# Optimization experiments

Hardware: AMD Instinct MI355X
Metric: run time of the kernel (lower is better)

The kernel has to match this reference:

```python
import jax, jax.numpy as jnp
import numpy as np

N_NODES = 100000
FIELD_DIM = 128
EMBED_DIM = 64
N_EDGES = 3200000
BATCH = 8192
NUM_FIELDS = 2


def setup_inputs() -> dict:
    key = jax.random.key(0)
    k1, k2, k3, k4 = jax.random.split(key, 4)
    features = jax.random.normal(k1, (N_NODES, FIELD_DIM), dtype=jnp.float32)
    edge_index = jax.random.randint(k2, (2, N_EDGES), 0, N_NODES, dtype=jnp.int32)
    # GCNConv linear weight (Glorot-ish scale) and bias
    W = jax.random.normal(k3, (FIELD_DIM, EMBED_DIM), dtype=jnp.float32) * (1.0 / np.sqrt(FIELD_DIM))
    bias = jnp.zeros((EMBED_DIM,), dtype=jnp.float32)
    x = jax.random.randint(k4, (BATCH, NUM_FIELDS), 0, N_NODES, dtype=jnp.int32)
    return {"features": features, "edge_index": edge_index, "W": W, "bias": bias, "x": x}


def reference(features, edge_index, W, bias, x):
    # GCNConv: out = D^{-1/2} (A + I) D^{-1/2} (X W) + b, then gather rows by x.
    n = features.shape[0]
    loop = jnp.arange(n, dtype=edge_index.dtype)
    src = jnp.concatenate([edge_index[0], loop])  # [E + N]
    dst = jnp.concatenate([edge_index[1], loop])  # [E + N]
    # degree (with self-loops) per destination node; >= 1 so rsqrt is safe
    deg = jax.ops.segment_sum(jnp.ones_like(dst, dtype=features.dtype), dst, num_segments=n)
    dinv = jax.lax.rsqrt(deg)
    norm = dinv[src] * dinv[dst]  # [E + N]
    h = features @ W  # [N, EMBED_DIM]
    msgs = h[src] * norm[:, None]  # gather + scale
    out = jax.ops.segment_sum(msgs, dst, num_segments=n) + bias  # [N, EMBED_DIM]
    return out[x]  # [BATCH, NUM_FIELDS, EMBED_DIM]
```

## Files before the change

kernel.cpp:

```cpp
#include <hip/hip_runtime.h>

#define N_NODES   100000
#define FIELD_DIM 128
#define EMBED_DIM 64
#define N_EDGES   3200000
#define NX        16384

#define NRANGE    4
#define RN        25000
#define RNH       12500
#define NSLICE    64
#define SLICE_E   (N_EDGES / NSLICE)
#define FILLB     (N_EDGES / 4 / 256)
#define GEMMB     ((N_NODES + 63) / 64)

typedef short  bf16x8 __attribute__((ext_vector_type(8)));
typedef float  f32x4  __attribute__((ext_vector_type(4)));

__device__ __forceinline__ unsigned short f2bf(float x) {
    unsigned u = __float_as_uint(x);
    u += 0x7FFF + ((u >> 16) & 1);
    return (unsigned short)(u >> 16);
}
__device__ __forceinline__ float bf2f(unsigned short b) {
    return __uint_as_float(((unsigned)b) << 16);
}
__device__ __forceinline__ unsigned pk2(float lo, float hi) {
    return (unsigned)f2bf(lo) | ((unsigned)f2bf(hi) << 16);
}

__global__ void k_zero(float4* __restrict__ z4) {
    int i = blockIdx.x * blockDim.x + threadIdx.x;
    if (i < 784) z4[i] = make_float4(0.f, 0.f, 0.f, 0.f);
}

__global__ void k_init(const int* __restrict__ x, unsigned int* __restrict__ bits,
                       const float* __restrict__ W, unsigned short* __restrict__ Wt) {
    int b = blockIdx.x;
    if (b < 64) {
        int i = b * 256 + threadIdx.x;
        int v = x[i];
        atomicOr(&bits[v >> 5], 1u << (v & 31));
    } else {
        for (int i = threadIdx.x; i < FIELD_DIM * EMBED_DIM; i += 256) {
            int k = i >> 6, c = i & 63;
            Wt[c * FIELD_DIM + k] = f2bf(W[i]);
        }
    }
}

__global__ __launch_bounds__(256) void k_hist(const int* __restrict__ dst,
                                              unsigned int* __restrict__ partial32) {
    __shared__ unsigned int hist[RNH];
    int tid = threadIdx.x;
    int q = blockIdx.x & 3, s = blockIdx.x >> 2;
    for (int i = tid; i < RNH; i += 256) hist[i] = 0;
    __syncthreads();
    int lo = q * RN;
    const int4* dp = (const int4*)(dst + s * SLICE_E);
    for (int i = tid; i < SLICE_E / 4; i += 256) {
        int4 d = dp[i];
        int a;
        a = d.x - lo; if ((unsigned)a < RN) atomicAdd(&hist[a >> 1], 1u << ((a & 1) << 4));
        a = d.y - lo; if ((unsigned)a < RN) atomicAdd(&hist[a >> 1], 1u << ((a & 1) << 4));
        a = d.z - lo; if ((unsigned)a < RN) atomicAdd(&hist[a >> 1], 1u << ((a & 1) << 4));
        a = d.w - lo; if ((unsigned)a < RN) atomicAdd(&hist[a >> 1], 1u << ((a & 1) << 4));
    }
    __syncthreads();
    unsigned int* po = partial32 + (size_t)blockIdx.x * RNH;
    for (int i = tid; i < RNH; i += 256) po[i] = hist[i];
}

__global__ __launch_bounds__(256) void k_reduce(const unsigned int* __restrict__ partial32,
                                                const unsigned int* __restrict__ bits,
                                                int* __restrict__ cnt,
                                                float* __restrict__ dinv,
                                                int* __restrict__ nlist,
                                                int* __restrict__ inv,
                                                int* __restrict__ off,
                                                int* __restrict__ cur,
                                                unsigned long long* __restrict__ counters) {
    __shared__ int wtot[4], wedge[4], ptot[4], pedge[4];
    __shared__ unsigned int baseN, baseE;
    int tid = threadIdx.x;
    int v = blockIdx.x * 256 + tid;
    bool inb = (v < N_NODES);
    int vc = inb ? v : (N_NODES - 1);
    int q = vc / RN, loc = vc - q * RN;
    int i2 = loc >> 1, sh = (loc & 1) << 4;
    const unsigned int* p = partial32 + (size_t)q * RNH + i2;
    int c = 0;
#pragma unroll
    for (int sb = 0; sb < 4; ++sb) {
        unsigned int vals[16];
#pragma unroll
        for (int s = 0; s < 16; ++s) vals[s] = p[(size_t)(sb * 16 + s) * (NRANGE * RNH)];
#pragma unroll
        for (int s = 0; s < 16; ++s) c += (int)((vals[s] >> sh) & 0xFFFFu);
    }
    if (inb) {
        cnt[v] = c;
        dinv[v] = rsqrtf((float)c + 1.0f);
    }
    bool fl = inb && ((bits[v >> 5] >> (v & 31)) & 1u);
    int lane = tid & 63;
    int w = tid >> 6;
    unsigned long long mask = __ballot(fl);
    int cc = fl ? c : 0;
    int incl = cc;
#pragma unroll
    for (int o = 1; o < 64; o <<= 1) {
        int t = __shfl_up(incl, o);
        if (lane >= o) incl += t;
    }
    if (lane == 63) { wtot[w] = __popcll(mask); wedge[w] = incl; }
    int myi = __popcll(mask & ((1ull << lane) - 1));
    int excl = incl - cc;
    __syncthreads();
    if (tid == 0) {
        int t0 = wtot[0], t1 = wtot[1], t2 = wtot[2], t3 = wtot[3];
        int e0 = wedge[0], e1 = wedge[1], e2 = wedge[2], e3 = wedge[3];
        ptot[0] = 0; ptot[1] = t0; ptot[2] = t0 + t1; ptot[3] = t0 + t1 + t2;
        pedge[0] = 0; pedge[1] = e0; pedge[2] = e0 + e1; pedge[3] = e0 + e1 + e2;
        int bt = t0 + t1 + t2 + t3;
        int be = e0 + e1 + e2 + e3;
        if (bt > 0) {
            unsigned long long add = ((unsigned long long)(unsigned)be << 32) |
                                     (unsigned long long)(unsigned)bt;
            unsigned long long old = atomicAdd(counters, add);
            baseN = (unsigned)(old & 0xFFFFFFFFull);
            baseE = (unsigned)(old >> 32);
        } else {
            baseN = 0; baseE = 0;
        }
    }
    __syncthreads();
    if (fl) {
        int i = (int)baseN + ptot[w] + myi;
        int o = (int)baseE + pedge[w] + excl;
        nlist[i] = v;
        inv[v] = i;
        off[v] = o;
        cur[v] = o;
    }
}

__global__ __launch_bounds__(256) void k_fillgemm(const int* __restrict__ src,
                                                  const int* __restrict__ dst,
                                                  const unsigned int* __restrict__ bits,
                                                  int* __restrict__ cur,
                                                  int* __restrict__ elist,
                                                  const float* __restrict__ F,
                                                  const unsigned short* __restrict__ Wt,
                                                  unsigned short* __restrict__ h) {
    if (blockIdx.x < FILLB) {
        int i = blockIdx.x * 256 + threadIdx.x;
        int4 d4 = ((const int4*)dst)[i];
        int4 s4 = ((const int4*)src)[i];
#define FILL1(dd, ss) if ((bits[(unsigned)(dd) >> 5] >> ((dd) & 31)) & 1u) \
        { int p = atomicAdd(&cur[dd], 1); elist[p] = ss; }
        FILL1(d4.x, s4.x)
        FILL1(d4.y, s4.y)
        FILL1(d4.z, s4.z)
        FILL1(d4.w, s4.w)
#undef FILL1
        return;
    }
    int gb = blockIdx.x - FILLB;
    int tid = threadIdx.x;
    int wave = tid >> 6, lane = tid & 63;
    int l15 = lane & 15, kg = lane >> 4;

    const char* wb = (const char*)Wt;
    bf16x8 bfrag[4][4];
#pragma unroll
    for (int cb = 0; cb < 4; ++cb)
#pragma unroll
        for (int ks = 0; ks < 4; ++ks)
            bfrag[cb][ks] = *(const bf16x8*)(wb + (cb * 16 + l15) * 256 + ks * 64 + kg * 16);

    int row = gb * 64 + wave * 16 + l15;
    int rowc = min(row, N_NODES - 1);
    const float4* F4 = (const float4*)(F + (size_t)rowc * FIELD_DIM + kg * 8);

    f32x4 acc[4];
#pragma unroll
    for (int cb = 0; cb < 4; ++cb) acc[cb] = (f32x4){0.f, 0.f, 0.f, 0.f};

#pragma unroll
    for (int ks = 0; ks < 4; ++ks) {
        float4 fa = F4[ks * 8];
        float4 fb = F4[ks * 8 + 1];
        union { bf16x8 v; unsigned u[4]; } af;
        af.u[0] = pk2(fa.x, fa.y);
        af.u[1] = pk2(fa.z, fa.w);
        af.u[2] = pk2(fb.x, fb.y);
        af.u[3] = pk2(fb.z, fb.w);
#pragma unroll
        for (int cb = 0; cb < 4; ++cb)
            acc[cb] = __builtin_amdgcn_mfma_f32_16x16x32_bf16(af.v, bfrag[cb][ks],
                                                              acc[cb], 0, 0, 0);
    }
    int rbase = gb * 64 + wave * 16 + kg * 4;
#pragma unroll
    for (int r = 0; r < 4; ++r) {
        int orow = rbase + r;
        if (orow < N_NODES) {
            unsigned short* hp = h + (size_t)orow * 64 + l15;
#pragma unroll
            for (int cb = 0; cb < 4; ++cb) hp[cb * 16] = f2bf(acc[cb][r]);
        }
    }
}

__global__ __launch_bounds__(256) void k_pull(const int* __restrict__ nlist,
                                              const int* __restrict__ counters,
                                              const int* __restrict__ cnt,
                                              const int* __restrict__ off,
                                              const int* __restrict__ elist,
                                              const unsigned short* __restrict__ h,
                                              const float* __restrict__ dinv,
                                              const float* __restrict__ bias,
                                              float* __restrict__ accc) {
    int t = blockIdx.x * blockDim.x + threadIdx.x;
    int wid = t >> 6;
    int lane = t & 63;
    if (wid >= counters[0]) return;
    int v = nlist[wid];
    float dvd = dinv[v];
    int deg = cnt[v];
    int base = off[v];
    float acc = bf2f(h[(size_t)v * 64 + lane]) * (dvd * dvd) + bias[lane];
    float acc2 = 0.f;
    int j = 0;
    for (; j + 7 < deg; j += 8) {
        int s0 = elist[base + j + 0];
        int s1 = elist[base + j + 1];
        int s2 = elist[base + j + 2];
        int s3 = elist[base + j + 3];
        int s4 = elist[base + j + 4];
        int s5 = elist[base + j + 5];
        int s6 = elist[base + j + 6];
        int s7 = elist[base + j + 7];
        float v0 = bf2f(h[(size_t)s0 * 64 + lane]);
        float v1 = bf2f(h[(size_t)s1 * 64 + lane]);
        float v2 = bf2f(h[(size_t)s2 * 64 + lane]);
        float v3 = bf2f(h[(size_t)s3 * 64 + lane]);
        float v4 = bf2f(h[(size_t)s4 * 64 + lane]);
        float v5 = bf2f(h[(size_t)s5 * 64 + lane]);
        float v6 = bf2f(h[(size_t)s6 * 64 + lane]);
        float v7 = bf2f(h[(size_t)s7 * 64 + lane]);
        float n0 = dinv[s0], n1 = dinv[s1], n2 = dinv[s2], n3 = dinv[s3];
        float n4 = dinv[s4], n5 = dinv[s5], n6 = dinv[s6], n7 = dinv[s7];
        acc  += v0 * (n0 * dvd);
        acc2 += v1 * (n1 * dvd);
        acc  += v2 * (n2 * dvd);
        acc2 += v3 * (n3 * dvd);
        acc  += v4 * (n4 * dvd);
        acc2 += v5 * (n5 * dvd);
        acc  += v6 * (n6 * dvd);
        acc2 += v7 * (n7 * dvd);
    }
    for (; j < deg; ++j) {
        int s0 = elist[base + j];
        acc += bf2f(h[(size_t)s0 * 64 + lane]) * (dinv[s0] * dvd);
    }
    accc[(size_t)wid * 64 + lane] = acc + acc2;
}

__global__ void k_gather(const int* __restrict__ x,
                         const int* __restrict__ inv,
                         const float* __restrict__ accc,
                         float* __restrict__ out) {
    int g = blockIdx.x * blockDim.x + threadIdx.x;
    if (g >= NX * 64) return;
    int v = x[g >> 6];
    out[g] = accc[(size_t)inv[v] * 64 + (g & 63)];
}

extern "C" void kernel_launch(void* const* d_in, const int* in_sizes, int n_in,
                              void* d_out, int out_size, void* d_ws, size_t ws_size,
                              hipStream_t stream) {
    const float* features = (const float*)d_in[0];
    const int*   edge     = (const int*)d_in[1];
    const float* W        = (const float*)d_in[2];
    const float* bias     = (const float*)d_in[3];
    const int*   x        = (const int*)d_in[4];
    float* out = (float*)d_out;

    char* ws = (char*)d_ws;
    unsigned short* h16      = (unsigned short*)(ws);
    unsigned int*   partial32= (unsigned int*)(ws + 12800000);
    int*            elist    = (int*)(ws + 12800000);
    float*          accc     = (float*)(ws + 25600000);
    int*            cnt      = (int*)  (ws + 29794304);
    float*          dinv     = (float*)(ws + 30194304);
    int*            off      = (int*)  (ws + 30594304);
    int*            inv      = (int*)  (ws + 30994304);
    int*            nlist    = (int*)  (ws + 31394304);
    int*            cur      = (int*)  (ws + 31459840);
    unsigned long long* counters = (unsigned long long*)(ws + 31859840);
    unsigned int*   bits     = (unsigned int*) (ws + 31859872);
    unsigned short* Wt       = (unsigned short*)(ws + 31872384);

    const int* esrc = edge;
    const int* edst = edge + N_EDGES;

    k_zero    <<<4, 256, 0, stream>>>((float4*)(ws + 31859840));
    k_init    <<<65, 256, 0, stream>>>(x, bits, W, Wt);
    k_hist    <<<NRANGE * NSLICE, 256, 0, stream>>>(edst, partial32);
    k_reduce  <<<(N_NODES + 255) / 256, 256, 0, stream>>>(partial32, bits, cnt, dinv,
                                                          nlist, inv, off, cur, counters);
    k_fillgemm<<<FILLB + GEMMB, 256, 0, stream>>>(esrc, edst, bits, cur, elist,
                                                  features, Wt, h16);
    k_pull    <<<(NX * 64 + 255) / 256, 256, 0, stream>>>(nlist, (const int*)counters,
                                                          cnt, off, elist, h16, dinv,
                                                          bias, accc);
    k_gather  <<<(NX * 64 + 255) / 256, 256, 0, stream>>>(x, inv, accc, out);
}
```

Baseline: 122.4 us.

## Co-schedule GEMM with histogram kernel and pad fill cursors per node

Moves the feature GEMM out of the edge-fill kernel and interleaves its blocks with the degree histogram blocks, one histogram block per seven. The fill kernel becomes standalone, and its per-node atomic cursors are spaced 64 bytes apart to reduce contention on shared cache lines. The trade-offs are a larger workspace footprint for the cursor array and the loss of the earlier overlap between the GEMM and the fill.

```diff
diff --git a/kernel.cpp b/kernel.cpp
--- a/kernel.cpp
+++ b/kernel.cpp
@@ -11,8 +11,9 @@
 #define RNH       12500
 #define NSLICE    64
 #define SLICE_E   (N_EDGES / NSLICE)
+#define HISTB     (NRANGE * NSLICE)
+#define GEMMB     ((N_NODES + 63) / 64)
 #define FILLB     (N_EDGES / 4 / 256)
-#define GEMMB     ((N_NODES + 63) / 64)
 
 typedef short  bf16x8 __attribute__((ext_vector_type(8)));
 typedef float  f32x4  __attribute__((ext_vector_type(4)));
@@ -49,26 +50,79 @@
     }
 }
 
-__global__ __launch_bounds__(256) void k_hist(const int* __restrict__ dst,
-                                              unsigned int* __restrict__ partial32) {
+__global__ __launch_bounds__(256) void k_histgemm(const int* __restrict__ dst,
+                                                  unsigned int* __restrict__ partial32,
+                                                  const float* __restrict__ F,
+                                                  const unsigned short* __restrict__ Wt,
+                                                  unsigned short* __restrict__ h) {
     __shared__ unsigned int hist[RNH];
+    int b = blockIdx.x;
     int tid = threadIdx.x;
-    int q = blockIdx.x & 3, s = blockIdx.x >> 2;
-    for (int i = tid; i < RNH; i += 256) hist[i] = 0;
-    __syncthreads();
-    int lo = q * RN;
-    const int4* dp = (const int4*)(dst + s * SLICE_E);
-    for (int i = tid; i < SLICE_E / 4; i += 256) {
-        int4 d = dp[i];
-        int a;
-        a = d.x - lo; if ((unsigned)a < RN) atomicAdd(&hist[a >> 1], 1u << ((a & 1) << 4));
-        a = d.y - lo; if ((unsigned)a < RN) atomicAdd(&hist[a >> 1], 1u << ((a & 1) << 4));
-        a = d.z - lo; if ((unsigned)a < RN) atomicAdd(&hist[a >> 1], 1u << ((a & 1) << 4));
-        a = d.w - lo; if ((unsigned)a < RN) atomicAdd(&hist[a >> 1], 1u << ((a & 1) << 4));
-    }
-    __syncthreads();
-    unsigned int* po = partial32 + (size_t)blockIdx.x * RNH;
-    for (int i = tid; i < RNH; i += 256) po[i] = hist[i];
+    bool ish = ((b % 7) == 0) && (b / 7 < HISTB);
+    if (ish) {
+        int hid = b / 7;
+        int q = hid & 3, s = hid >> 2;
+        for (int i = tid; i < RNH; i += 256) hist[i] = 0;
+        __syncthreads();
+        int lo = q * RN;
+        const int4* dp = (const int4*)(dst + s * SLICE_E);
+        for (int i = tid; i < SLICE_E / 4; i += 256) {
+            int4 d = dp[i];
+            int a;
+            a = d.x - lo; if ((unsigned)a < RN) atomicAdd(&hist[a >> 1], 1u << ((a & 1) << 4));
+            a = d.y - lo; if ((unsigned)a < RN) atomicAdd(&hist[a >> 1], 1u << ((a & 1) << 4));
+            a = d.z - lo; if ((unsigned)a < RN) atomicAdd(&hist[a >> 1], 1u << ((a & 1) << 4));
+            a = d.w - lo; if ((unsigned)a < RN) atomicAdd(&hist[a >> 1], 1u << ((a & 1) << 4));
+        }
+        __syncthreads();
+        unsigned int* po = partial32 + (size_t)hid * RNH;
+        for (int i = tid; i < RNH; i += 256) po[i] = hist[i];
+        return;
+    }
+    int gb = b - min((b + 6) / 7, HISTB);
+    int wave = tid >> 6, lane = tid & 63;
+    int l15 = lane & 15, kg = lane >> 4;
+
+    const char* wb = (const char*)Wt;
+    bf16x8 bfrag[4][4];
+#pragma unroll
+    for (int cb = 0; cb < 4; ++cb)
+#pragma unroll
+        for (int ks = 0; ks < 4; ++ks)
+            bfrag[cb][ks] = *(const bf16x8*)(wb + (cb * 16 + l15) * 256 + ks * 64 + kg * 16);
+
+    int row = gb * 64 + wave * 16 + l15;
+    int rowc = min(row, N_NODES - 1);
+    const float4* F4 = (const float4*)(F + (size_t)rowc * FIELD_DIM + kg * 8);
+
+    f32x4 acc[4];
+#pragma unroll
+    for (int cb = 0; cb < 4; ++cb) acc[cb] = (f32x4){0.f, 0.f, 0.f, 0.f};
+
+#pragma unroll
+    for (int ks = 0; ks < 4; ++ks) {
+        float4 fa = F4[ks * 8];
+        float4 fb = F4[ks * 8 + 1];
+        union { bf16x8 v; unsigned u[4]; } af;
+        af.u[0] = pk2(fa.x, fa.y);
+        af.u[1] = pk2(fa.z, fa.w);
+        af.u[2] = pk2(fb.x, fb.y);
+        af.u[3] = pk2(fb.z, fb.w);
+#pragma unroll
+        for (int cb = 0; cb < 4; ++cb)
+            acc[cb] = __builtin_amdgcn_mfma_f32_16x16x32_bf16(af.v, bfrag[cb][ks],
+                                                              acc[cb], 0, 0, 0);
+    }
+    int rbase = gb * 64 + wave * 16 + kg * 4;
+#pragma unroll
+    for (int r = 0; r < 4; ++r) {
+        int orow = rbase + r;
+        if (orow < N_NODES) {
+            unsigned short* hp = h + (size_t)orow * 64 + l15;
+#pragma unroll
+            for (int cb = 0; cb < 4; ++cb) hp[cb * 16] = f2bf(acc[cb][r]);
+        }
+    }
 }
 
 __global__ __launch_bounds__(256) void k_reduce(const unsigned int* __restrict__ partial32,
@@ -78,7 +132,7 @@
                                                 int* __restrict__ nlist,
                                                 int* __restrict__ inv,
                                                 int* __restrict__ off,
-                                                int* __restrict__ cur,
+                                                int* __restrict__ cur16,
                                                 unsigned long long* __restrict__ counters) {
     __shared__ int wtot[4], wedge[4], ptot[4], pedge[4];
     __shared__ unsigned int baseN, baseE;
@@ -141,76 +195,25 @@
         nlist[i] = v;
         inv[v] = i;
         off[v] = o;
-        cur[v] = o;
-    }
-}
-
-__global__ __launch_bounds__(256) void k_fillgemm(const int* __restrict__ src,
-                                                  const int* __restrict__ dst,
-                                                  const unsigned int* __restrict__ bits,
-                                                  int* __restrict__ cur,
-                                                  int* __restrict__ elist,
-                                                  const float* __restrict__ F,
-                                                  const unsigned short* __restrict__ Wt,
-                                                  unsigned short* __restrict__ h) {
-    if (blockIdx.x < FILLB) {
-        int i = blockIdx.x * 256 + threadIdx.x;
-        int4 d4 = ((const int4*)dst)[i];
-        int4 s4 = ((const int4*)src)[i];
+        cur16[v << 4] = o;
+    }
+}
+
+__global__ __launch_bounds__(256) void k_fill(const int* __restrict__ src,
+                                              const int* __restrict__ dst,
+                                              const unsigned int* __restrict__ bits,
+                                              int* __restrict__ cur16,
+                                              int* __restrict__ elist) {
+    int i = blockIdx.x * 256 + threadIdx.x;
+    int4 d4 = ((const int4*)dst)[i];
+    int4 s4 = ((const int4*)src)[i];
 #define FILL1(dd, ss) if ((bits[(unsigned)(dd) >> 5] >> ((dd) & 31)) & 1u) \
-        { int p = atomicAdd(&cur[dd], 1); elist[p] = ss; }
-        FILL1(d4.x, s4.x)
-        FILL1(d4.y, s4.y)
-        FILL1(d4.z, s4.z)
-        FILL1(d4.w, s4.w)
+    { int p = atomicAdd(&cur16[(dd) << 4], 1); elist[p] = ss; }
+    FILL1(d4.x, s4.x)
+    FILL1(d4.y, s4.y)
+    FILL1(d4.z, s4.z)
+    FILL1(d4.w, s4.w)
 #undef FILL1
-        return;
-    }
-    int gb = blockIdx.x - FILLB;
-    int tid = threadIdx.x;
-    int wave = tid >> 6, lane = tid & 63;
-    int l15 = lane & 15, kg = lane >> 4;
-
-    const char* wb = (const char*)Wt;
-    bf16x8 bfrag[4][4];
-#pragma unroll
-    for (int cb = 0; cb < 4; ++cb)
-#pragma unroll
-        for (int ks = 0; ks < 4; ++ks)
-            bfrag[cb][ks] = *(const bf16x8*)(wb + (cb * 16 + l15) * 256 + ks * 64 + kg * 16);
-
-    int row = gb * 64 + wave * 16 + l15;
-    int rowc = min(row, N_NODES - 1);
-    const float4* F4 = (const float4*)(F + (size_t)rowc * FIELD_DIM + kg * 8);
-
-    f32x4 acc[4];
-#pragma unroll
-    for (int cb = 0; cb < 4; ++cb) acc[cb] = (f32x4){0.f, 0.f, 0.f, 0.f};
-
-#pragma unroll
-    for (int ks = 0; ks < 4; ++ks) {
-        float4 fa = F4[ks * 8];
-        float4 fb = F4[ks * 8 + 1];
-        union { bf16x8 v; unsigned u[4]; } af;
-        af.u[0] = pk2(fa.x, fa.y);
-        af.u[1] = pk2(fa.z, fa.w);
-        af.u[2] = pk2(fb.x, fb.y);
-        af.u[3] = pk2(fb.z, fb.w);
-#pragma unroll
-        for (int cb = 0; cb < 4; ++cb)
-            acc[cb] = __builtin_amdgcn_mfma_f32_16x16x32_bf16(af.v, bfrag[cb][ks],
-                                                              acc[cb], 0, 0, 0);
-    }
-    int rbase = gb * 64 + wave * 16 + kg * 4;
-#pragma unroll
-    for (int r = 0; r < 4; ++r) {
-        int orow = rbase + r;
-        if (orow < N_NODES) {
-            unsigned short* hp = h + (size_t)orow * 64 + l15;
-#pragma unroll
-            for (int cb = 0; cb < 4; ++cb) hp[cb * 16] = f2bf(acc[cb][r]);
-        }
-    }
 }
 
 __global__ __launch_bounds__(256) void k_pull(const int* __restrict__ nlist,
@@ -298,21 +301,20 @@
     int*            off      = (int*)  (ws + 30594304);
     int*            inv      = (int*)  (ws + 30994304);
     int*            nlist    = (int*)  (ws + 31394304);
-    int*            cur      = (int*)  (ws + 31459840);
-    unsigned long long* counters = (unsigned long long*)(ws + 31859840);
-    unsigned int*   bits     = (unsigned int*) (ws + 31859872);
-    unsigned short* Wt       = (unsigned short*)(ws + 31872384);
+    unsigned long long* counters = (unsigned long long*)(ws + 31459840);
+    unsigned int*   bits     = (unsigned int*) (ws + 31459872);
+    unsigned short* Wt       = (unsigned short*)(ws + 31472384);
+    int*            cur16    = (int*)  (ws + 31488768);
 
     const int* esrc = edge;
     const int* edst = edge + N_EDGES;
 
-    k_zero    <<<4, 256, 0, stream>>>((float4*)(ws + 31859840));
+    k_zero    <<<4, 256, 0, stream>>>((float4*)(ws + 31459840));
     k_init    <<<65, 256, 0, stream>>>(x, bits, W, Wt);
-    k_hist    <<<NRANGE * NSLICE, 256, 0, stream>>>(edst, partial32);
+    k_histgemm<<<HISTB + GEMMB, 256, 0, stream>>>(edst, partial32, features, Wt, h16);
     k_reduce  <<<(N_NODES + 255) / 256, 256, 0, stream>>>(partial32, bits, cnt, dinv,
-                                                          nlist, inv, off, cur, counters);
-    k_fillgemm<<<FILLB + GEMMB, 256, 0, stream>>>(esrc, edst, bits, cur, elist,
-                                                  features, Wt, h16);
+                                                          nlist, inv, off, cur16, counters);
+    k_fill    <<<FILLB, 256, 0, stream>>>(esrc, edst, bits, cur16, elist);
     k_pull    <<<(NX * 64 + 255) / 256, 256, 0, stream>>>(nlist, (const int*)counters,
                                                           cnt, off, elist, h16, dinv,
                                                           bias, accc);
```

New measurement: 121.3 us. About the same (-0.9%).

## Interleave fill and GEMM blocks, pad atomic cursors, widen histogram slicing

Applied to the files above, without the earlier changes.

The edge-histogram kernel now uses 125 slices instead of 64, launching more blocks, and each thread issues five vectorized loads before its shared-memory atomics. The fill/GEMM kernel interleaves one GEMM block between every two fill blocks instead of placing all GEMM blocks after the fill blocks, so compute-bound and atomic-bound work share the GPU. The per-node fill cursors are spread to one per 64-byte stride to cut atomic contention on shared cache lines. The workspace layout is moved to fit the larger partial-histogram buffer and the padded cursor array, which uses more memory and more reduce reads.

```diff
diff --git a/kernel.cpp b/kernel.cpp
--- a/kernel.cpp
+++ b/kernel.cpp
@@ -9,10 +9,11 @@
 #define NRANGE    4
 #define RN        25000
 #define RNH       12500
-#define NSLICE    64
+#define NSLICE    125
 #define SLICE_E   (N_EDGES / NSLICE)
+#define HISTB     (NRANGE * NSLICE)
+#define GEMMB     ((N_NODES + 63) / 64)
 #define FILLB     (N_EDGES / 4 / 256)
-#define GEMMB     ((N_NODES + 63) / 64)
 
 typedef short  bf16x8 __attribute__((ext_vector_type(8)));
 typedef float  f32x4  __attribute__((ext_vector_type(4)));
@@ -58,13 +59,19 @@
     __syncthreads();
     int lo = q * RN;
     const int4* dp = (const int4*)(dst + s * SLICE_E);
-    for (int i = tid; i < SLICE_E / 4; i += 256) {
-        int4 d = dp[i];
-        int a;
-        a = d.x - lo; if ((unsigned)a < RN) atomicAdd(&hist[a >> 1], 1u << ((a & 1) << 4));
-        a = d.y - lo; if ((unsigned)a < RN) atomicAdd(&hist[a >> 1], 1u << ((a & 1) << 4));
-        a = d.z - lo; if ((unsigned)a < RN) atomicAdd(&hist[a >> 1], 1u << ((a & 1) << 4));
-        a = d.w - lo; if ((unsigned)a < RN) atomicAdd(&hist[a >> 1], 1u << ((a & 1) << 4));
+#pragma unroll
+    for (int bt = 0; bt < 5; ++bt) {
+        int4 d[5];
+#pragma unroll
+        for (int u = 0; u < 5; ++u) d[u] = dp[tid + 256 * (bt * 5 + u)];
+#pragma unroll
+        for (int u = 0; u < 5; ++u) {
+            int a;
+            a = d[u].x - lo; if ((unsigned)a < RN) atomicAdd(&hist[a >> 1], 1u << ((a & 1) << 4));
+            a = d[u].y - lo; if ((unsigned)a < RN) atomicAdd(&hist[a >> 1], 1u << ((a & 1) << 4));
+            a = d[u].z - lo; if ((unsigned)a < RN) atomicAdd(&hist[a >> 1], 1u << ((a & 1) << 4));
+            a = d[u].w - lo; if ((unsigned)a < RN) atomicAdd(&hist[a >> 1], 1u << ((a & 1) << 4));
+        }
     }
     __syncthreads();
     unsigned int* po = partial32 + (size_t)blockIdx.x * RNH;
@@ -78,7 +85,7 @@
                                                 int* __restrict__ nlist,
                                                 int* __restrict__ inv,
                                                 int* __restrict__ off,
-                                                int* __restrict__ cur,
+                                                int* __restrict__ cur16,
                                                 unsigned long long* __restrict__ counters) {
     __shared__ int wtot[4], wedge[4], ptot[4], pedge[4];
     __shared__ unsigned int baseN, baseE;
@@ -91,12 +98,12 @@
     const unsigned int* p = partial32 + (size_t)q * RNH + i2;
     int c = 0;
 #pragma unroll
-    for (int sb = 0; sb < 4; ++sb) {
-        unsigned int vals[16];
-#pragma unroll
-        for (int s = 0; s < 16; ++s) vals[s] = p[(size_t)(sb * 16 + s) * (NRANGE * RNH)];
-#pragma unroll
-        for (int s = 0; s < 16; ++s) c += (int)((vals[s] >> sh) & 0xFFFFu);
+    for (int sb = 0; sb < 5; ++sb) {
+        unsigned int vals[25];
+#pragma unroll
+        for (int s = 0; s < 25; ++s) vals[s] = p[(size_t)(sb * 25 + s) * (NRANGE * RNH)];
+#pragma unroll
+        for (int s = 0; s < 25; ++s) c += (int)((vals[s] >> sh) & 0xFFFFu);
     }
     if (inb) {
         cnt[v] = c;
@@ -141,24 +148,28 @@
         nlist[i] = v;
         inv[v] = i;
         off[v] = o;
-        cur[v] = o;
+        cur16[v << 4] = o;
     }
 }
 
 __global__ __launch_bounds__(256) void k_fillgemm(const int* __restrict__ src,
                                                   const int* __restrict__ dst,
                                                   const unsigned int* __restrict__ bits,
-                                                  int* __restrict__ cur,
+                                                  int* __restrict__ cur16,
                                                   int* __restrict__ elist,
                                                   const float* __restrict__ F,
                                                   const unsigned short* __restrict__ Wt,
                                                   unsigned short* __restrict__ h) {
-    if (blockIdx.x < FILLB) {
-        int i = blockIdx.x * 256 + threadIdx.x;
+    int b = blockIdx.x;
+    int tid = threadIdx.x;
+    bool isg = ((b % 3) == 0) && (b / 3 < GEMMB);
+    if (!isg) {
+        int fb = b - min(b / 3 + 1, GEMMB);
+        int i = fb * 256 + tid;
         int4 d4 = ((const int4*)dst)[i];
         int4 s4 = ((const int4*)src)[i];
 #define FILL1(dd, ss) if ((bits[(unsigned)(dd) >> 5] >> ((dd) & 31)) & 1u) \
-        { int p = atomicAdd(&cur[dd], 1); elist[p] = ss; }
+        { int p = atomicAdd(&cur16[(dd) << 4], 1); elist[p] = ss; }
         FILL1(d4.x, s4.x)
         FILL1(d4.y, s4.y)
         FILL1(d4.z, s4.z)
@@ -166,8 +177,7 @@
 #undef FILL1
         return;
     }
-    int gb = blockIdx.x - FILLB;
-    int tid = threadIdx.x;
+    int gb = b / 3;
     int wave = tid >> 6, lane = tid & 63;
     int l15 = lane & 15, kg = lane >> 4;
 
@@ -292,26 +302,26 @@
     unsigned short* h16      = (unsigned short*)(ws);
     unsigned int*   partial32= (unsigned int*)(ws + 12800000);
     int*            elist    = (int*)(ws + 12800000);
-    float*          accc     = (float*)(ws + 25600000);
-    int*            cnt      = (int*)  (ws + 29794304);
-    float*          dinv     = (float*)(ws + 30194304);
-    int*            off      = (int*)  (ws + 30594304);
-    int*            inv      = (int*)  (ws + 30994304);
-    int*            nlist    = (int*)  (ws + 31394304);
-    int*            cur      = (int*)  (ws + 31459840);
-    unsigned long long* counters = (unsigned long long*)(ws + 31859840);
-    unsigned int*   bits     = (unsigned int*) (ws + 31859872);
-    unsigned short* Wt       = (unsigned short*)(ws + 31872384);
+    float*          accc     = (float*)(ws + 37800000);
+    int*            cnt      = (int*)  (ws + 41994304);
+    float*          dinv     = (float*)(ws + 42394304);
+    int*            off      = (int*)  (ws + 42794304);
+    int*            inv      = (int*)  (ws + 43194304);
+    int*            nlist    = (int*)  (ws + 43594304);
+    unsigned long long* counters = (unsigned long long*)(ws + 43659840);
+    unsigned int*   bits     = (unsigned int*) (ws + 43659872);
+    unsigned short* Wt       = (unsigned short*)(ws + 43672384);
+    int*            cur16    = (int*)  (ws + 43688768);
 
     const int* esrc = edge;
     const int* edst = edge + N_EDGES;
 
-    k_zero    <<<4, 256, 0, stream>>>((float4*)(ws + 31859840));
+    k_zero    <<<4, 256, 0, stream>>>((float4*)(ws + 43659840));
     k_init    <<<65, 256, 0, stream>>>(x, bits, W, Wt);
-    k_hist    <<<NRANGE * NSLICE, 256, 0, stream>>>(edst, partial32);
+    k_hist    <<<HISTB, 256, 0, stream>>>(edst, partial32);
     k_reduce  <<<(N_NODES + 255) / 256, 256, 0, stream>>>(partial32, bits, cnt, dinv,
-                                                          nlist, inv, off, cur, counters);
-    k_fillgemm<<<FILLB + GEMMB, 256, 0, stream>>>(esrc, edst, bits, cur, elist,
+                                                          nlist, inv, off, cur16, counters);
+    k_fillgemm<<<FILLB + GEMMB, 256, 0, stream>>>(esrc, edst, bits, cur16, elist,
                                                   features, Wt, h16);
     k_pull    <<<(NX * 64 + 255) / 256, 256, 0, stream>>>(nlist, (const int*)counters,
                                                           cnt, off, elist, h16, dinv,
```

Result: faster. 104.7 us (-14.5%).
